# Kernel optimization log

Hardware: AMD Instinct MI355X
Metric: run time of the kernel (lower is better)

## Reference

```python
import jax, jax.numpy as jnp
import numpy as np

K = 31   # avg_pool2d kernel_size
PAD = 15 # avg_pool2d padding (count_include_pad=True -> divide by K*K always)


def box_mean(x):
    # x: (N, C, H, W). Zero-padded 31x31 box filter, stride 1, same output size.
    s = jax.lax.reduce_window(
        x, 0.0, jax.lax.add,
        window_dimensions=(1, 1, K, K),
        window_strides=(1, 1, 1, 1),
        padding=((0, 0), (0, 0), (PAD, PAD), (PAD, PAD)))
    return s / (K * K)


def setup_inputs() -> dict:
    key = jax.random.key(0)
    k1, k2 = jax.random.split(key)
    N, C, H, W = 16, 2, 512, 512
    pred = jax.random.normal(k1, (N, C, H, W), dtype=jnp.float32)
    target = jax.random.randint(k2, (N, H, W), 0, C)  # class labels in [0, C)
    return {"pred": pred, "target": target}


def reference(pred, target):
    LOSS_WEIGHT = 1.0
    N, C, H, W = pred.shape
    # _expand_onehot_labels: clamp to [0, C], one-hot C+1, drop last, NHWC->NCHW
    t = jnp.clip(target, 0, C)
    mask = jnp.transpose(jax.nn.one_hot(t, C + 1, dtype=pred.dtype)[..., :C],
                         (0, 3, 1, 2))  # (N, C, H, W), float
    # ignore_index=255 > C so the channel filter keeps all channels (no-op)

    weit = 1.0 + 5.0 * jnp.abs(box_mean(mask) - mask)

    # F.binary_cross_entropy_with_logits(pred, mask, reduce='none'):
    # legacy `reduce='none'` is truthy -> reduction='mean' in torch, so wbce is
    # the GLOBAL mean of elementwise BCE; the subsequent weighted normalization
    # (weit*wbce).sum/weit.sum is then an identity broadcast. Replicated faithfully.
    bce = jnp.maximum(pred, 0.0) - pred * mask + jnp.log1p(jnp.exp(-jnp.abs(pred)))
    wbce = jnp.mean(bce)  # scalar

    p = jax.nn.sigmoid(pred)
    inter = jnp.sum(p * mask * weit, axis=(2, 3))          # (N, C)
    union = jnp.sum((p + mask) * weit, axis=(2, 3))        # (N, C)
    wiou = 1.0 - (inter + 1.0) / (union - inter + 1.0)     # (N, C)

    return LOSS_WEIGHT * jnp.mean(wbce + wiou)
```

## Files before the change

kernel.cpp:

```cpp
#include <hip/hip_runtime.h>
#include <stdint.h>

#define N_IMG 16
#define H_DIM 512
#define W_DIM 512
#define PADR 15
#define BAND 8
#define HALO (BAND + 2 * PADR)
#define WPR 18
#define NBANDS (H_DIM / BAND)
#define WROW (W_DIM / 32)


__global__ __launch_bounds__(256) void bitmap_kernel(const int4* __restrict__ tg4,
                                                     uint32_t* __restrict__ bm) {
    const int tid = threadIdx.x;
    const size_t t = (size_t)blockIdx.x * 256 + tid;
    const int4 a = tg4[t * 2];
    const int4 b = tg4[t * 2 + 1];
    uint32_t by = (uint32_t)(a.x == 1) | ((uint32_t)(a.y == 1) << 1) |
                  ((uint32_t)(a.z == 1) << 2) | ((uint32_t)(a.w == 1) << 3) |
                  ((uint32_t)(b.x == 1) << 4) | ((uint32_t)(b.y == 1) << 5) |
                  ((uint32_t)(b.z == 1) << 6) | ((uint32_t)(b.w == 1) << 7);
    uint32_t w = by << (8 * (tid & 3));
    w |= __shfl_xor(w, 1);
    w |= __shfl_xor(w, 2);
    if ((tid & 3) == 0) bm[t >> 2] = w;
}

__global__ __launch_bounds__(512, 8) void mega_kernel(const uint32_t* __restrict__ bm,
                                                      const float* __restrict__ pred,
                                                      float* __restrict__ part) {
    __shared__ uint32_t B[HALO][WPR];
    const int tid = threadIdx.x;
    const int band = blockIdx.x;
    const int n = blockIdx.y;
    const int r0 = band * BAND;
    const int col = tid;

    const uint32_t* __restrict__ bmn = bm + (size_t)n * H_DIM * WROW;
    const int hr0 = tid >> 4, wi = tid & 15;
    const int ra = r0 - PADR + hr0;
    uint32_t w0 = 0, w1 = 0;
    if (ra >= 0 && ra < H_DIM) w0 = bmn[ra * WROW + wi];
    const int hr1 = hr0 + 32;
    const int rb = r0 - PADR + hr1;
    if (tid < 96 && rb >= 0 && rb < H_DIM) w1 = bmn[rb * WROW + wi];

    const size_t img = (size_t)n * H_DIM * W_DIM;
    const float* __restrict__ p0 = pred + img * 2 + (size_t)r0 * W_DIM + col;
    const float* __restrict__ p1 = p0 + (size_t)H_DIM * W_DIM;
    float x0[BAND], x1[BAND];
#pragma unroll
    for (int rr = 0; rr < BAND; ++rr) {
        x0[rr] = p0[rr * W_DIM];
        x1[rr] = p1[rr * W_DIM];
    }

    if (tid < 2 * HALO) B[tid >> 1][(tid & 1) ? (WPR - 1) : 0] = 0u;
    B[hr0][1 + wi] = w0;
    if (tid < 96) B[hr1][1 + wi] = w1;
    __syncthreads();

    const int b = col + (32 - PADR);
    const int q = b >> 5, s = b & 31;
    uint32_t run = 0, mbits = 0;
    uint32_t hlo[7], hhi[7];
#pragma unroll
    for (int i = 0; i < HALO; ++i) {
        const uint32_t lo = B[i][q];
        const uint32_t hi = B[i][q + 1];
        const uint32_t val =
            (uint32_t)((((uint64_t)hi << 32) | lo) >> s) & 0x7FFFFFFFu;
        const uint32_t hv = (uint32_t)__popc(val);
        if (i < 31) run += hv;
        if (i < 7) hlo[i] = hv;
        if (i >= 31) hhi[i - 31] = hv;
        if (i >= PADR && i < PADR + BAND)
            mbits |= ((val >> PADR) & 1u) << (i - PADR);
    }

#pragma unroll
    for (int rr = 0; rr < BAND; ++rr) asm volatile("" : "+v"(x0[rr]), "+v"(x1[rr]));
#pragma unroll
    for (int i = 0; i < 7; ++i) asm volatile("" : "+v"(hlo[i]), "+v"(hhi[i]));

    const int cntw = min(col + PADR, W_DIM - 1) - max(col - PADR, 0) + 1;
    const float inv961 = 1.0f / 961.0f;
    float bce = 0.f, in0 = 0.f, in1 = 0.f, un0 = 0.f, un1 = 0.f;

#pragma unroll
    for (int rr = 0; rr < BAND; ++rr) {
        const int r = r0 + rr;
        const int cnth = min(r + PADR, H_DIM - 1) - max(r - PADR, 0) + 1;
        const float cnt = (float)(cnth * cntw);
        const float m1 = (float)((mbits >> rr) & 1u);
        const float m0 = 1.0f - m1;
        const float V = (float)run;
        const float box1 = V * inv961;
        const float box0 = (cnt - V) * inv961;
        const float w1f = 1.0f + 5.0f * fabsf(box1 - m1);
        const float w0f = 1.0f + 5.0f * fabsf(box0 - m0);
        {
            const float x = x0[rr];
            const float t = __expf(-fabsf(x));
            const float inv = __builtin_amdgcn_rcpf(1.0f + t);
            const float p = (x >= 0.f) ? inv : t * inv;
            bce += fmaxf(x, 0.f) - x * m0 + __logf(1.0f + t);
            in0 += p * m0 * w0f;
            un0 += (p + m0) * w0f;
        }
        {
            const float x = x1[rr];
            const float t = __expf(-fabsf(x));
            const float inv = __builtin_amdgcn_rcpf(1.0f + t);
            const float p = (x >= 0.f) ? inv : t * inv;
            bce += fmaxf(x, 0.f) - x * m1 + __logf(1.0f + t);
            in1 += p * m1 * w1f;
            un1 += (p + m1) * w1f;
        }
        if (rr < BAND - 1)
            run += hhi[rr] - hlo[rr];
    }

    __shared__ float red[8 * 5];
    const int lane = tid & 63, wv = tid >> 6;
    float v[5] = {bce, in0, in1, un0, un1};
#pragma unroll
    for (int k = 0; k < 5; ++k)
#pragma unroll
        for (int off = 32; off > 0; off >>= 1)
            v[k] += __shfl_down(v[k], off);
    if (lane == 0)
#pragma unroll
        for (int k = 0; k < 5; ++k) red[wv * 5 + k] = v[k];
    __syncthreads();
    if (tid == 0) {
        float s2[5];
#pragma unroll
        for (int k = 0; k < 5; ++k) {
            s2[k] = red[k];
            for (int w2 = 1; w2 < 8; ++w2) s2[k] += red[w2 * 5 + k];
        }
        float* p = part + (size_t)(n * NBANDS + band) * 5;
#pragma unroll
        for (int k = 0; k < 5; ++k) p[k] = s2[k];
    }
}

__global__ __launch_bounds__(256) void finalize_kernel(const float* __restrict__ part,
                                                       float* __restrict__ out) {
    const int tid = threadIdx.x;
    const int n = tid >> 4;
    const int i = tid & 15;
    float bce = 0.f, in0 = 0.f, in1 = 0.f, un0 = 0.f, un1 = 0.f;
#pragma unroll
    for (int j = 0; j < 4; ++j) {
        const float* p = part + (size_t)(n * NBANDS + j * 16 + i) * 5;
        bce += p[0]; in0 += p[1]; in1 += p[2]; un0 += p[3]; un1 += p[4];
    }
#pragma unroll
    for (int off = 8; off > 0; off >>= 1) {
        bce += __shfl_xor(bce, off, 16);
        in0 += __shfl_xor(in0, off, 16);
        in1 += __shfl_xor(in1, off, 16);
        un0 += __shfl_xor(un0, off, 16);
        un1 += __shfl_xor(un1, off, 16);
    }
    __shared__ float fb[16], fw[16];
    if (i == 0) {
        fb[n] = bce;
        fw[n] = (1.0f - (in0 + 1.0f) / (un0 - in0 + 1.0f)) +
                (1.0f - (in1 + 1.0f) / (un1 - in1 + 1.0f));
    }
    __syncthreads();
    if (tid == 0) {
        float sb = 0.f, sw = 0.f;
#pragma unroll
        for (int k = 0; k < 16; ++k) { sb += fb[k]; sw += fw[k]; }
        out[0] = sb / 8388608.0f + sw * (1.0f / 32.0f);
    }
}

extern "C" void kernel_launch(void* const* d_in, const int* in_sizes, int n_in,
                              void* d_out, int out_size, void* d_ws, size_t ws_size,
                              hipStream_t stream) {
    const float* pred = (const float*)d_in[0];
    const int* target = (const int*)d_in[1];
    float* part = (float*)d_ws;
    uint32_t* bm = (uint32_t*)((char*)d_ws + 32768);

    bitmap_kernel<<<2048, 256, 0, stream>>>((const int4*)target, bm);
    dim3 grid(NBANDS, N_IMG);
    mega_kernel<<<grid, 512, 0, stream>>>(bm, pred, part);
    finalize_kernel<<<1, 256, 0, stream>>>(part, (float*)d_out);
}
```

Baseline: 24.74 us.

## Process two columns per thread over 16-row bands with shared popcount windows

```diff
diff --git a/kernel.cpp b/kernel.cpp
--- a/kernel.cpp
+++ b/kernel.cpp
@@ -5,10 +5,10 @@
 #define H_DIM 512
 #define W_DIM 512
 #define PADR 15
-#define BAND 8
+#define BAND 16
 #define HALO (BAND + 2 * PADR)
 #define WPR 18
-#define NBANDS (H_DIM / BAND)
+#define NBANDS 32
 #define WROW (W_DIM / 32)
 
 
@@ -28,7 +28,7 @@
     if ((tid & 3) == 0) bm[t >> 2] = w;
 }
 
-__global__ __launch_bounds__(512, 8) void mega_kernel(const uint32_t* __restrict__ bm,
+__global__ __launch_bounds__(512, 4) void mega_kernel(const uint32_t* __restrict__ bm,
                                                       const float* __restrict__ pred,
                                                       float* __restrict__ part) {
     __shared__ uint32_t B[HALO][WPR];
@@ -36,73 +36,75 @@
     const int band = blockIdx.x;
     const int n = blockIdx.y;
     const int r0 = band * BAND;
-    const int col = tid;
+    const int cg = tid & 255, rg = tid >> 8;
+    const int c0 = cg * 2;
 
     const uint32_t* __restrict__ bmn = bm + (size_t)n * H_DIM * WROW;
-    const int hr0 = tid >> 4, wi = tid & 15;
-    const int ra = r0 - PADR + hr0;
-    uint32_t w0 = 0, w1 = 0;
-    if (ra >= 0 && ra < H_DIM) w0 = bmn[ra * WROW + wi];
-    const int hr1 = hr0 + 32;
-    const int rb = r0 - PADR + hr1;
-    if (tid < 96 && rb >= 0 && rb < H_DIM) w1 = bmn[rb * WROW + wi];
+    const int hrA = tid >> 4, wiA = tid & 15;
+    const int ra = r0 - PADR + hrA;
+    uint32_t wA = 0, wB = 0;
+    if (ra >= 0 && ra < H_DIM) wA = bmn[ra * WROW + wiA];
+    const int hrB = 32 + (tid >> 4);
+    const int rb = r0 - PADR + hrB;
+    if (tid < 224 && rb >= 0 && rb < H_DIM) wB = bmn[rb * WROW + wiA];
 
     const size_t img = (size_t)n * H_DIM * W_DIM;
-    const float* __restrict__ p0 = pred + img * 2 + (size_t)r0 * W_DIM + col;
+    const float* __restrict__ p0 = pred + img * 2 + (size_t)(r0 + rg * 8) * W_DIM + c0;
     const float* __restrict__ p1 = p0 + (size_t)H_DIM * W_DIM;
-    float x0[BAND], x1[BAND];
-#pragma unroll
-    for (int rr = 0; rr < BAND; ++rr) {
-        x0[rr] = p0[rr * W_DIM];
-        x1[rr] = p1[rr * W_DIM];
+    float2 x0[8], x1[8];
+#pragma unroll
+    for (int rr = 0; rr < 8; ++rr) {
+        x0[rr] = *reinterpret_cast<const float2*>(p0 + rr * W_DIM);
+        x1[rr] = *reinterpret_cast<const float2*>(p1 + rr * W_DIM);
     }
 
     if (tid < 2 * HALO) B[tid >> 1][(tid & 1) ? (WPR - 1) : 0] = 0u;
-    B[hr0][1 + wi] = w0;
-    if (tid < 96) B[hr1][1 + wi] = w1;
+    B[hrA][1 + wiA] = wA;
+    if (tid < 224) B[hrB][1 + wiA] = wB;
     __syncthreads();
 
-    const int b = col + (32 - PADR);
-    const int q = b >> 5, s = b & 31;
-    uint32_t run = 0, mbits = 0;
-    uint32_t hlo[7], hhi[7];
-#pragma unroll
-    for (int i = 0; i < HALO; ++i) {
-        const uint32_t lo = B[i][q];
-        const uint32_t hi = B[i][q + 1];
-        const uint32_t val =
-            (uint32_t)((((uint64_t)hi << 32) | lo) >> s) & 0x7FFFFFFFu;
-        const uint32_t hv = (uint32_t)__popc(val);
-        if (i < 31) run += hv;
-        if (i < 7) hlo[i] = hv;
-        if (i >= 31) hhi[i - 31] = hv;
-        if (i >= PADR && i < PADR + BAND)
-            mbits |= ((val >> PADR) & 1u) << (i - PADR);
-    }
-
-#pragma unroll
-    for (int rr = 0; rr < BAND; ++rr) asm volatile("" : "+v"(x0[rr]), "+v"(x1[rr]));
-#pragma unroll
-    for (int i = 0; i < 7; ++i) asm volatile("" : "+v"(hlo[i]), "+v"(hhi[i]));
-
-    const int cntw = min(col + PADR, W_DIM - 1) - max(col - PADR, 0) + 1;
+    const int b0 = c0 + (32 - PADR);
+    const int q = b0 >> 5, s = b0 & 31;
+    uint32_t run0 = 0, run1 = 0, mb0 = 0, mb1 = 0;
+    uint32_t hlo0[7], hlo1[7], hhi0[7], hhi1[7];
+#pragma unroll
+    for (int i = 0; i < 38; ++i) {
+        const int j = rg * 8 + i;
+        const uint32_t lo = B[j][q];
+        const uint32_t hi = B[j][q + 1];
+        const uint32_t w32 = (uint32_t)((((uint64_t)hi << 32) | lo) >> s);
+        const uint32_t h0 = (uint32_t)__popc(w32 & 0x7FFFFFFFu);
+        const uint32_t h1 = (uint32_t)__popc(w32 >> 1);
+        if (i < 31) { run0 += h0; run1 += h1; }
+        if (i < 7) { hlo0[i] = h0; hlo1[i] = h1; }
+        if (i >= 31) { hhi0[i - 31] = h0; hhi1[i - 31] = h1; }
+        if (i >= PADR && i < PADR + 8) {
+            mb0 |= ((w32 >> 15) & 1u) << (i - PADR);
+            mb1 |= ((w32 >> 16) & 1u) << (i - PADR);
+        }
+    }
+
+#pragma unroll
+    for (int rr = 0; rr < 8; ++rr)
+        asm volatile("" : "+v"(x0[rr].x), "+v"(x0[rr].y), "+v"(x1[rr].x), "+v"(x1[rr].y));
+#pragma unroll
+    for (int i = 0; i < 7; ++i)
+        asm volatile("" : "+v"(hlo0[i]), "+v"(hlo1[i]), "+v"(hhi0[i]), "+v"(hhi1[i]));
+
+    const float cw0 = (float)(min(c0 + PADR, W_DIM - 1) - max(c0 - PADR, 0) + 1);
+    const float cw1 = (float)(min(c0 + 1 + PADR, W_DIM - 1) - max(c0 + 1 - PADR, 0) + 1);
     const float inv961 = 1.0f / 961.0f;
     float bce = 0.f, in0 = 0.f, in1 = 0.f, un0 = 0.f, un1 = 0.f;
 
-#pragma unroll
-    for (int rr = 0; rr < BAND; ++rr) {
-        const int r = r0 + rr;
-        const int cnth = min(r + PADR, H_DIM - 1) - max(r - PADR, 0) + 1;
-        const float cnt = (float)(cnth * cntw);
-        const float m1 = (float)((mbits >> rr) & 1u);
+    auto docol = [&](float xc0, float xc1, uint32_t V, uint32_t mbit, float cnt) {
+        const float m1 = (float)mbit;
         const float m0 = 1.0f - m1;
-        const float V = (float)run;
-        const float box1 = V * inv961;
-        const float box0 = (cnt - V) * inv961;
+        const float box1 = (float)V * inv961;
+        const float box0 = (cnt - (float)V) * inv961;
         const float w1f = 1.0f + 5.0f * fabsf(box1 - m1);
         const float w0f = 1.0f + 5.0f * fabsf(box0 - m0);
         {
-            const float x = x0[rr];
+            const float x = xc0;
             const float t = __expf(-fabsf(x));
             const float inv = __builtin_amdgcn_rcpf(1.0f + t);
             const float p = (x >= 0.f) ? inv : t * inv;
@@ -111,7 +113,7 @@
             un0 += (p + m0) * w0f;
         }
         {
-            const float x = x1[rr];
+            const float x = xc1;
             const float t = __expf(-fabsf(x));
             const float inv = __builtin_amdgcn_rcpf(1.0f + t);
             const float p = (x >= 0.f) ? inv : t * inv;
@@ -119,8 +121,18 @@
             in1 += p * m1 * w1f;
             un1 += (p + m1) * w1f;
         }
-        if (rr < BAND - 1)
-            run += hhi[rr] - hlo[rr];
+    };
+
+#pragma unroll
+    for (int rr = 0; rr < 8; ++rr) {
+        const int r = r0 + rg * 8 + rr;
+        const float cnth = (float)(min(r + PADR, H_DIM - 1) - max(r - PADR, 0) + 1);
+        docol(x0[rr].x, x1[rr].x, run0, (mb0 >> rr) & 1u, cnth * cw0);
+        docol(x0[rr].y, x1[rr].y, run1, (mb1 >> rr) & 1u, cnth * cw1);
+        if (rr < 7) {
+            run0 += hhi0[rr] - hlo0[rr];
+            run1 += hhi1[rr] - hlo1[rr];
+        }
     }
 
     __shared__ float red[8 * 5];
@@ -155,7 +167,7 @@
     const int i = tid & 15;
     float bce = 0.f, in0 = 0.f, in1 = 0.f, un0 = 0.f, un1 = 0.f;
 #pragma unroll
-    for (int j = 0; j < 4; ++j) {
+    for (int j = 0; j < 2; ++j) {
         const float* p = part + (size_t)(n * NBANDS + j * 16 + i) * 5;
         bce += p[0]; in0 += p[1]; in1 += p[2]; un0 += p[3]; un1 += p[4];
     }
```

New measurement: 46.85 us. 89.3% more time.

## Precompute horizontal box counts per pixel in first pass, drop shared bitmap

Applied to the files above, without the earlier changes.

```diff
diff --git a/kernel.cpp b/kernel.cpp
--- a/kernel.cpp
+++ b/kernel.cpp
@@ -9,43 +9,62 @@
 #define HALO (BAND + 2 * PADR)
 #define WPR 18
 #define NBANDS (H_DIM / BAND)
-#define WROW (W_DIM / 32)
 
 
-__global__ __launch_bounds__(256) void bitmap_kernel(const int4* __restrict__ tg4,
-                                                     uint32_t* __restrict__ bm) {
+__global__ __launch_bounds__(256) void hrow_kernel(const int4* __restrict__ tg4,
+                                                   uint8_t* __restrict__ hb) {
+    __shared__ uint32_t B[4][WPR];
     const int tid = threadIdx.x;
     const size_t t = (size_t)blockIdx.x * 256 + tid;
     const int4 a = tg4[t * 2];
-    const int4 b = tg4[t * 2 + 1];
-    uint32_t by = (uint32_t)(a.x == 1) | ((uint32_t)(a.y == 1) << 1) |
-                  ((uint32_t)(a.z == 1) << 2) | ((uint32_t)(a.w == 1) << 3) |
-                  ((uint32_t)(b.x == 1) << 4) | ((uint32_t)(b.y == 1) << 5) |
-                  ((uint32_t)(b.z == 1) << 6) | ((uint32_t)(b.w == 1) << 7);
+    const int4 b4 = tg4[t * 2 + 1];
+    const uint32_t by = (uint32_t)(a.x == 1) | ((uint32_t)(a.y == 1) << 1) |
+                        ((uint32_t)(a.z == 1) << 2) | ((uint32_t)(a.w == 1) << 3) |
+                        ((uint32_t)(b4.x == 1) << 4) | ((uint32_t)(b4.y == 1) << 5) |
+                        ((uint32_t)(b4.z == 1) << 6) | ((uint32_t)(b4.w == 1) << 7);
     uint32_t w = by << (8 * (tid & 3));
     w |= __shfl_xor(w, 1);
     w |= __shfl_xor(w, 2);
-    if ((tid & 3) == 0) bm[t >> 2] = w;
+    if (tid < 8) B[tid >> 1][(tid & 1) ? (WPR - 1) : 0] = 0u;
+    const int widx = tid >> 2;
+    if ((tid & 3) == 0) B[widx >> 4][1 + (widx & 15)] = w;
+    __syncthreads();
+
+    const int p0 = tid * 8;
+    const int row = p0 >> 9;
+    const int c0 = p0 & 511;
+    const int bb = c0 + 17;
+    const int q = bb >> 5, s0 = bb & 31;
+    const uint32_t lo = B[row][q], hi = B[row][q + 1];
+    const uint64_t dw = ((uint64_t)hi << 32) | lo;
+    uint32_t pk0 = 0, pk1 = 0;
+#pragma unroll
+    for (int k = 0; k < 4; ++k) {
+        const uint32_t v0 = (uint32_t)(dw >> (s0 + k)) & 0x7FFFFFFFu;
+        const uint32_t v1 = (uint32_t)(dw >> (s0 + 4 + k)) & 0x7FFFFFFFu;
+        pk0 |= ((uint32_t)__popc(v0) | (((by >> k) & 1u) << 7)) << (8 * k);
+        pk1 |= ((uint32_t)__popc(v1) | (((by >> (4 + k)) & 1u) << 7)) << (8 * k);
+    }
+    *reinterpret_cast<uint2*>(hb + (size_t)blockIdx.x * 2048 + p0) =
+        make_uint2(pk0, pk1);
 }
 
-__global__ __launch_bounds__(512, 8) void mega_kernel(const uint32_t* __restrict__ bm,
+__global__ __launch_bounds__(512, 8) void mega_kernel(const uint8_t* __restrict__ hb,
                                                       const float* __restrict__ pred,
                                                       float* __restrict__ part) {
-    __shared__ uint32_t B[HALO][WPR];
     const int tid = threadIdx.x;
     const int band = blockIdx.x;
     const int n = blockIdx.y;
     const int r0 = band * BAND;
     const int col = tid;
+    const uint8_t* __restrict__ hn = hb + (size_t)n * H_DIM * W_DIM;
 
-    const uint32_t* __restrict__ bmn = bm + (size_t)n * H_DIM * WROW;
-    const int hr0 = tid >> 4, wi = tid & 15;
-    const int ra = r0 - PADR + hr0;
-    uint32_t w0 = 0, w1 = 0;
-    if (ra >= 0 && ra < H_DIM) w0 = bmn[ra * WROW + wi];
-    const int hr1 = hr0 + 32;
-    const int rb = r0 - PADR + hr1;
-    if (tid < 96 && rb >= 0 && rb < H_DIM) w1 = bmn[rb * WROW + wi];
+    uint32_t bv[HALO];
+#pragma unroll
+    for (int i = 0; i < HALO; ++i) {
+        const int r = r0 - PADR + i;
+        bv[i] = (r >= 0 && r < H_DIM) ? (uint32_t)hn[(size_t)r * W_DIM + col] : 0u;
+    }
 
     const size_t img = (size_t)n * H_DIM * W_DIM;
     const float* __restrict__ p0 = pred + img * 2 + (size_t)r0 * W_DIM + col;
@@ -57,33 +76,14 @@
         x1[rr] = p1[rr * W_DIM];
     }
 
-    if (tid < 2 * HALO) B[tid >> 1][(tid & 1) ? (WPR - 1) : 0] = 0u;
-    B[hr0][1 + wi] = w0;
-    if (tid < 96) B[hr1][1 + wi] = w1;
-    __syncthreads();
-
-    const int b = col + (32 - PADR);
-    const int q = b >> 5, s = b & 31;
     uint32_t run = 0, mbits = 0;
-    uint32_t hlo[7], hhi[7];
 #pragma unroll
-    for (int i = 0; i < HALO; ++i) {
-        const uint32_t lo = B[i][q];
-        const uint32_t hi = B[i][q + 1];
-        const uint32_t val =
-            (uint32_t)((((uint64_t)hi << 32) | lo) >> s) & 0x7FFFFFFFu;
-        const uint32_t hv = (uint32_t)__popc(val);
-        if (i < 31) run += hv;
-        if (i < 7) hlo[i] = hv;
-        if (i >= 31) hhi[i - 31] = hv;
-        if (i >= PADR && i < PADR + BAND)
-            mbits |= ((val >> PADR) & 1u) << (i - PADR);
-    }
+    for (int i = 0; i < 31; ++i) run += bv[i] & 0x7Fu;
+#pragma unroll
+    for (int rr = 0; rr < BAND; ++rr) mbits |= (bv[PADR + rr] >> 7) << rr;
 
 #pragma unroll
     for (int rr = 0; rr < BAND; ++rr) asm volatile("" : "+v"(x0[rr]), "+v"(x1[rr]));
-#pragma unroll
-    for (int i = 0; i < 7; ++i) asm volatile("" : "+v"(hlo[i]), "+v"(hhi[i]));
 
     const int cntw = min(col + PADR, W_DIM - 1) - max(col - PADR, 0) + 1;
     const float inv961 = 1.0f / 961.0f;
@@ -120,7 +120,7 @@
             un1 += (p + m1) * w1f;
         }
         if (rr < BAND - 1)
-            run += hhi[rr] - hlo[rr];
+            run += (bv[rr + 31] & 0x7Fu) - (bv[rr] & 0x7Fu);
     }
 
     __shared__ float red[8 * 5];
@@ -188,10 +188,10 @@
     const float* pred = (const float*)d_in[0];
     const int* target = (const int*)d_in[1];
     float* part = (float*)d_ws;
-    uint32_t* bm = (uint32_t*)((char*)d_ws + 32768);
+    uint8_t* hb = (uint8_t*)d_ws + 32768;
 
-    bitmap_kernel<<<2048, 256, 0, stream>>>((const int4*)target, bm);
+    hrow_kernel<<<2048, 256, 0, stream>>>((const int4*)target, hb);
     dim3 grid(NBANDS, N_IMG);
-    mega_kernel<<<grid, 512, 0, stream>>>(bm, pred, part);
+    mega_kernel<<<grid, 512, 0, stream>>>(hb, pred, part);
     finalize_kernel<<<1, 256, 0, stream>>>(part, (float*)d_out);
 }
```

New measurement: 35.51 us. +43.5%, slower.
